# Kernel optimization log

Hardware: AMD Instinct MI355X
Metric: run time of the kernel (lower is better)

## Reference

```python
import jax, jax.numpy as jnp
import numpy as np

B, T, H, W, CIN = 8, 10, 64, 64, 32
F = 64          # filters
KH, KW = 3, 3
G = 4           # num_gate_copies


def _conv(x, k):
    # x: (N,H,W,Cin), k: (kh,kw,Cin,Cout), SAME padding, stride 1
    return jax.lax.conv_general_dilated(
        x, k, window_strides=(1, 1), padding='SAME',
        dimension_numbers=('NHWC', 'HWIO', 'NHWC'))


def setup_inputs() -> dict:
    key = jax.random.key(0)
    k1, k2, k3, k4 = jax.random.split(key, 4)
    inputs = jax.random.normal(k1, (B, T, H, W, CIN), dtype=jnp.float32)
    label_values = jax.random.randint(k2, (B,), 0, G, dtype=jnp.int32)
    kernel = jax.random.normal(k3, (KH, KW, CIN, 4 * F), dtype=jnp.float32) * 0.05
    recurrent_kernel = jax.random.normal(k4, (G, KH, KW, F, 4 * F), dtype=jnp.float32) * 0.05
    # unit_forget_bias: zeros with forget-gate slice set to 1.0
    bias = jnp.zeros((G, 4 * F), dtype=jnp.float32).at[:, F:2 * F].set(1.0)
    return {"inputs": inputs, "label_values": label_values,
            "kernel": kernel, "recurrent_kernel": recurrent_kernel, "bias": bias}


def reference(inputs, label_values, kernel, recurrent_kernel, bias):
    b, t, h_dim, w_dim, _ = inputs.shape
    f = recurrent_kernel.shape[-1] // 4
    # Per-sample gather of expert recurrent kernel / bias (label-indexed)
    k_b = recurrent_kernel[label_values]   # (B, kh, kw, F, 4F)
    b_b = bias[label_values]               # (B, 4F)

    # vmapped per-sample batch=1 recurrent conv (faithful to map_fn semantics)
    per_sample_conv = jax.vmap(lambda hs, ks: _conv(hs[None], ks)[0])

    def step(carry, x_t):
        h, c = carry
        z = _conv(x_t, kernel) + per_sample_conv(h, k_b) + b_b[:, None, None, :]
        i = jax.nn.sigmoid(z[..., :f])
        fg = jax.nn.sigmoid(z[..., f:2 * f])
        g = jnp.tanh(z[..., 2 * f:3 * f])
        o = jax.nn.sigmoid(z[..., 3 * f:])
        c_new = fg * c + i * g
        h_new = o * jnp.tanh(c_new)
        return (h_new, c_new), h_new

    h0 = jnp.zeros((b, h_dim, w_dim, f), dtype=inputs.dtype)
    c0 = jnp.zeros_like(h0)
    xs = jnp.moveaxis(inputs, 1, 0)  # (T, B, H, W, Cin)
    _, ys = jax.lax.scan(step, (h0, c0), xs)
    return jnp.moveaxis(ys, 0, 1)    # (B, T, H, W, F)
```

## Files before the change

kernel.cpp:

```cpp
#include <hip/hip_runtime.h>


typedef __attribute__((ext_vector_type(8))) short short8v;
typedef __attribute__((ext_vector_type(4))) float f32x4;
typedef __attribute__((ext_vector_type(4))) unsigned int u32x4;
typedef unsigned short u16;

#define HS 808
#define HB 3200

__device__ __forceinline__ u16 f2bf(float x) {
    union { float f; unsigned u; } a; a.f = x;
    unsigned r = a.u + 0x7FFFu + ((a.u >> 16) & 1u);
    return (u16)(r >> 16);
}
__device__ __forceinline__ float sigf(float x) { return 1.0f / (1.0f + __expf(-x)); }
__device__ __forceinline__ float tanhf_(float x) {
    float e = __expf(2.0f * x);
    return 1.0f - 2.0f / (e + 1.0f);
}

__global__ __launch_bounds__(256)
void prep_w(const float* __restrict__ kern, const float* __restrict__ rk,
            u16* __restrict__ wt_in, u16* __restrict__ wt_rk,
            unsigned* __restrict__ flags) {
    int idx = blockIdx.x * 256 + threadIdx.x;
    if (idx < 512) flags[idx] = 0u;
    if (idx >= 82944) return;
    const float* s;
    u16* dst;
    if (idx < 9216) {
        int co = idx & 255, ckb = idx >> 8;
        int tap = ckb >> 2, kb = ckb & 3;
        s = kern + (size_t)((tap << 5) + (kb << 3)) * 256 + co;
        dst = wt_in + (size_t)idx * 8;
    } else {
        int j = idx - 9216;
        int co = j & 255, rest = j >> 8;
        int kb = rest & 3, gc = rest >> 2;
        int g = gc / 18, cc = gc - g * 18;
        int tap = cc >> 1;
        int cib = (cc & 1) << 5;
        s = rk + (size_t)(((g * 9 + tap) << 6) + cib + (kb << 3)) * 256 + co;
        dst = wt_rk + (size_t)j * 8;
    }
    union { u16 u[8]; uint4 q; } o;
    #pragma unroll
    for (int i = 0; i < 8; ++i) o.u[i] = f2bf(s[i * 256]);
    *(uint4*)dst = o.q;
}

__device__ __forceinline__ void stageXf(const float* __restrict__ src,
                                        short* __restrict__ halX,
                                        int tid, int y0, int x0) {
    #pragma unroll 2
    for (int s = tid; s < 400; s += 256) {
        int pos = s >> 2, kb = s & 3;
        int hy = pos / 10, hx = pos - hy * 10;
        int gy = y0 + hy - 1, gx = x0 + hx - 1;
        union { u16 u[8]; short8v v; } o;
        o.v = (short8v){0,0,0,0,0,0,0,0};
        if ((unsigned)gy < 64u && (unsigned)gx < 64u) {
            const float* p = src + (((gy << 6) + gx) << 5) + (kb << 3);
            float4 a0 = *(const float4*)p;
            float4 a1 = *(const float4*)(p + 4);
            o.u[0] = f2bf(a0.x); o.u[1] = f2bf(a0.y);
            o.u[2] = f2bf(a0.z); o.u[3] = f2bf(a0.w);
            o.u[4] = f2bf(a1.x); o.u[5] = f2bf(a1.y);
            o.u[6] = f2bf(a1.z); o.u[7] = f2bf(a1.w);
        }
        *(short8v*)&halX[kb * 800 + pos * 8] = o.v;
    }
}

__global__ __launch_bounds__(256, 2)
void lstm_all(const float* __restrict__ xf,
              const u16* __restrict__ wt_in, const u16* __restrict__ wt_rk,
              const float* __restrict__ bias, const int* __restrict__ labels,
              u16* __restrict__ hb0, u16* __restrict__ hb1,
              float* __restrict__ out, unsigned* __restrict__ flags)
{
    __shared__ short hal[HB + 8 * HS];

    const int tid  = threadIdx.x;
    const int lane = tid & 63;
    const int wq   = tid >> 6;
    const int b    = blockIdx.x >> 6;
    const int tile = blockIdx.x & 63;
    const int ty = tile >> 3, tx = tile & 7;
    const int y0 = ty << 3, x0 = tx << 3;
    const int g = labels[b];

    const int co_l = lane & 15;
    const int kbl  = lane >> 4;
    const int prow = (lane & 15) >> 3, pcol = lane & 7;
    const int f = (wq << 4) + co_l;

    float bv[4];
    #pragma unroll
    for (int n = 0; n < 4; ++n)
        bv[n] = bias[(g << 8) + (n << 6) + f];

    int aoffm[4];
    #pragma unroll
    for (int m = 0; m < 4; ++m)
        aoffm[m] = ((m << 1) + prow) * 10 + pcol;

    int poff[4][4], loff[4][4];
    #pragma unroll
    for (int m = 0; m < 4; ++m)
        #pragma unroll
        for (int rr = 0; rr < 4; ++rr) {
            int pf = (kbl << 2) + rr;
            int ly = (m << 1) + (pf >> 3);
            int lx = pf & 7;
            poff[m][rr] = ((((y0 + ly) << 6) + x0 + lx) << 6) + f;
            loff[m][rr] = HB + (f >> 3) * HS + ((ly + 1) * 10 + lx + 1) * 8 + (f & 7);
        }

    float cst[4][4];
    #pragma unroll
    for (int m = 0; m < 4; ++m)
        #pragma unroll
        for (int rr = 0; rr < 4; ++rr) cst[m][rr] = 0.0f;

    const float* xsrc = xf + ((size_t)b * 10 << 17);
    float*       ob0  = out + ((size_t)b * 10 << 18);
    unsigned*    myfl = flags + (b << 6) + tile;

    for (int s = tid; s < 808; s += 256)
        *(short8v*)&hal[HB + s * 8] = (short8v){0,0,0,0,0,0,0,0};
    stageXf(xsrc, hal, tid, y0, x0);
    __syncthreads();

    for (int t = 0; t < 10; ++t) {
        u16* hw = ((t & 1) ? hb1 : hb0) + ((size_t)b << 18);

        f32x4 acc[4][4];
        #pragma unroll
        for (int n = 0; n < 4; ++n)
            #pragma unroll
            for (int m = 0; m < 4; ++m)
                acc[m][n] = (f32x4){bv[n], bv[n], bv[n], bv[n]};

        #pragma unroll 3
        for (int tap = 0; tap < 9; ++tap) {
            const int koff = (tap / 3) * 10 + (tap % 3);
            const u16* wb = wt_in + (size_t)((((tap << 2) + kbl) << 8) + f) * 8;
            short8v bfr[4], af[4];
            #pragma unroll
            for (int n = 0; n < 4; ++n)
                bfr[n] = *(const short8v*)&wb[(size_t)n << 9];
            #pragma unroll
            for (int m = 0; m < 4; ++m)
                af[m] = *(const short8v*)&hal[kbl * 800 + (aoffm[m] + koff) * 8];
            #pragma unroll
            for (int m = 0; m < 4; ++m)
                #pragma unroll
                for (int n = 0; n < 4; ++n)
                    acc[m][n] = __builtin_amdgcn_mfma_f32_16x16x32_bf16(af[m], bfr[n], acc[m][n], 0, 0, 0);
        }

        if (t > 0) {
            if (tid < 64) {
                bool valid = false; int fidx = 0;
                if (tid < 8) {
                    int kk = tid + (tid >= 4);
                    int nty = ty + kk / 3 - 1, ntx = tx + kk % 3 - 1;
                    valid = (unsigned)nty < 8u && (unsigned)ntx < 8u;
                    fidx = (b << 6) + (nty << 3) + ntx;
                }
                unsigned tgt = (unsigned)t;
                int guard = 0;
                for (;;) {
                    unsigned vv = tgt;
                    if (valid)
                        vv = __hip_atomic_load(flags + fidx, __ATOMIC_RELAXED,
                                               __HIP_MEMORY_SCOPE_SYSTEM);
                    if (__all(vv >= tgt)) break;
                    if (++guard > (1 << 19)) break;
                    __builtin_amdgcn_s_sleep(2);
                }
            }
            __syncthreads();

            {
                const u16* hr = ((t & 1) ? hb0 : hb1) + ((size_t)b << 18);
                #pragma unroll
                for (int u = 0; u < 2; ++u) {
                    int s = tid + (u << 8);
                    if (s < 288) {
                        int posr = s >> 3, kb = s & 7;
                        int hy, hx;
                        if (posr < 10)      { hy = 0; hx = posr; }
                        else if (posr < 20) { hy = 9; hx = posr - 10; }
                        else { int v = posr - 20; hy = 1 + (v >> 1); hx = (v & 1) * 9; }
                        int gy = y0 + hy - 1, gx = x0 + hx - 1;
                        bool inb = (unsigned)gy < 64u && (unsigned)gx < 64u;
                        const u16* ga = inb ? (hr + (((gy << 6) + gx) << 6) + (kb << 3)) : hr;
                        u32x4 v;
                        asm volatile("global_load_dwordx4 %0, %1, off sc0 sc1"
                                     : "=v"(v) : "v"(ga) : "memory");
                        asm volatile("s_waitcnt vmcnt(0)" ::: "memory");
                        __builtin_amdgcn_sched_barrier(0);
                        if (!inb) v = (u32x4){0u, 0u, 0u, 0u};
                        *(u32x4*)&hal[HB + kb * HS + (hy * 10 + hx) * 8] = v;
                    }
                }
            }
            __syncthreads();

            #pragma unroll 3
            for (int c = 0; c < 18; ++c) {
                const int tap = c >> 1;
                const int koff = (tap / 3) * 10 + (tap % 3);
                const u16* wb = wt_rk + (size_t)(((((g * 18 + c) << 2) + kbl) << 8) + f) * 8;
                short8v bfr[4], af[4];
                #pragma unroll
                for (int n = 0; n < 4; ++n)
                    bfr[n] = *(const short8v*)&wb[(size_t)n << 9];
                const int abase = HB + (((c & 1) << 2) + kbl) * HS;
                #pragma unroll
                for (int m = 0; m < 4; ++m)
                    af[m] = *(const short8v*)&hal[abase + (aoffm[m] + koff) * 8];
                #pragma unroll
                for (int m = 0; m < 4; ++m)
                    #pragma unroll
                    for (int n = 0; n < 4; ++n)
                        acc[m][n] = __builtin_amdgcn_mfma_f32_16x16x32_bf16(af[m], bfr[n], acc[m][n], 0, 0, 0);
            }
        }
        __syncthreads();

        float* ob = ob0 + ((size_t)t << 18);
        #pragma unroll
        for (int m = 0; m < 4; ++m) {
            #pragma unroll
            for (int rr = 0; rr < 4; ++rr) {
                float zi = acc[m][0][rr], zf = acc[m][1][rr];
                float zg = acc[m][2][rr], zo = acc[m][3][rr];
                float cn = sigf(zf) * cst[m][rr] + sigf(zi) * tanhf_(zg);
                float hn = sigf(zo) * tanhf_(cn);
                cst[m][rr] = cn;
                ob[poff[m][rr]] = hn;
                hal[loff[m][rr]] = (short)f2bf(hn);
            }
        }
        __syncthreads();

        if (t < 9) {
            if (tid < 224) {
                int pxr = tid >> 3, kb = tid & 7;
                int dy, dx;
                if (pxr < 8)       { dy = 0; dx = pxr; }
                else if (pxr < 16) { dy = 7; dx = pxr - 8; }
                else { int v = pxr - 16; dy = 1 + (v >> 1); dx = (v & 1) * 7; }
                u32x4 v = *(const u32x4*)&hal[HB + kb * HS + ((dy + 1) * 10 + dx + 1) * 8];
                const u16* ga = hw + ((((y0 + dy) << 6) + x0 + dx) << 6) + (kb << 3);
                asm volatile("global_store_dwordx4 %0, %1, off sc0 sc1"
                             :: "v"(ga), "v"(v) : "memory");
            }
            stageXf(xsrc + ((size_t)(t + 1) << 17), hal, tid, y0, x0);
            asm volatile("s_waitcnt vmcnt(0)" ::: "memory");
            __syncthreads();
            if (tid == 0)
                __hip_atomic_fetch_add(myfl, 1u, __ATOMIC_RELAXED,
                                       __HIP_MEMORY_SCOPE_SYSTEM);
        }
    }
}

extern "C" void kernel_launch(void* const* d_in, const int* in_sizes, int n_in,
                              void* d_out, int out_size, void* d_ws, size_t ws_size,
                              hipStream_t stream)
{
    const float* x    = (const float*)d_in[0];
    const int*   lbl  = (const int*)  d_in[1];
    const float* kern = (const float*)d_in[2];
    const float* rk   = (const float*)d_in[3];
    const float* bias = (const float*)d_in[4];
    float* out = (float*)d_out;

    u16* hb0   = (u16*)d_ws;
    u16* hb1   = hb0 + 2097152;
    u16* wt_in = hb1 + 2097152;
    u16* wt_rk = wt_in + 73728;
    unsigned* flags = (unsigned*)(wt_rk + 589824);

    hipLaunchKernelGGL(prep_w, dim3(324), dim3(256), 0, stream,
                       kern, rk, wt_in, wt_rk, flags);

    hipLaunchKernelGGL(lstm_all, dim3(512), dim3(256), 0, stream,
                       x, wt_in, wt_rk, bias, lbl, hb0, hb1, out, flags);
}
```

Baseline: 172.1 us.

## Overlap halo neighbor loads with input-conv MFMA taps after flag wait

Splits the input convolution into two chunks and places the flag spin-wait between them. The halo reads of neighbouring h tiles are issued as relaxed atomic 64-bit loads before the last four input taps, so their global latency is hidden behind MFMA work. The old path serialized each load with a vmcnt(0) wait. Halo address offsets are now precomputed once outside the time loop. The risk is that more input-conv work sits after the wait, which could lengthen the critical path if the neighbour flags arrive early.

```diff
diff --git a/kernel.cpp b/kernel.cpp
--- a/kernel.cpp
+++ b/kernel.cpp
@@ -5,6 +5,7 @@
 typedef __attribute__((ext_vector_type(4))) float f32x4;
 typedef __attribute__((ext_vector_type(4))) unsigned int u32x4;
 typedef unsigned short u16;
+typedef unsigned long long u64;
 
 #define HS 808
 #define HB 3200
@@ -73,6 +74,26 @@
     }
 }
 
+__device__ __forceinline__ void xchunk(const u16* __restrict__ wt_in,
+                                       const short* __restrict__ hal,
+                                       f32x4 acc[4][4], const int* aoffm,
+                                       int tap, int kbl, int f) {
+    const int koff = (tap / 3) * 10 + (tap % 3);
+    const u16* wb = wt_in + (size_t)((((tap << 2) + kbl) << 8) + f) * 8;
+    short8v bfr[4], af[4];
+    #pragma unroll
+    for (int n = 0; n < 4; ++n)
+        bfr[n] = *(const short8v*)&wb[(size_t)n << 9];
+    #pragma unroll
+    for (int m = 0; m < 4; ++m)
+        af[m] = *(const short8v*)&hal[kbl * 800 + (aoffm[m] + koff) * 8];
+    #pragma unroll
+    for (int m = 0; m < 4; ++m)
+        #pragma unroll
+        for (int n = 0; n < 4; ++n)
+            acc[m][n] = __builtin_amdgcn_mfma_f32_16x16x32_bf16(af[m], bfr[n], acc[m][n], 0, 0, 0);
+}
+
 __global__ __launch_bounds__(256, 2)
 void lstm_all(const float* __restrict__ xf,
               const u16* __restrict__ wt_in, const u16* __restrict__ wt_rk,
@@ -118,6 +139,32 @@
             loff[m][rr] = HB + (f >> 3) * HS + ((ly + 1) * 10 + lx + 1) * 8 + (f & 7);
         }
 
+    int ilA, ilB = 0;
+    bool inA, inB = false;
+    const bool okB = tid < 32;
+    long offA = 0, offB = 0;
+    {
+        int posr = tid >> 3, kb = tid & 7;
+        int hy, hx;
+        if (posr < 10)      { hy = 0; hx = posr; }
+        else if (posr < 20) { hy = 9; hx = posr - 10; }
+        else { int v = posr - 20; hy = 1 + (v >> 1); hx = (v & 1) * 9; }
+        int gy = y0 + hy - 1, gx = x0 + hx - 1;
+        inA = (unsigned)gy < 64u && (unsigned)gx < 64u;
+        offA = inA ? (long)((((gy << 6) + gx) << 6) + (kb << 3)) : 0;
+        ilA = HB + kb * HS + (hy * 10 + hx) * 8;
+    }
+    if (okB) {
+        int s = tid + 256;
+        int posr = s >> 3, kb = s & 7;
+        int v = posr - 20;
+        int hy = 1 + (v >> 1), hx = (v & 1) * 9;
+        int gy = y0 + hy - 1, gx = x0 + hx - 1;
+        inB = (unsigned)gy < 64u && (unsigned)gx < 64u;
+        offB = inB ? (long)((((gy << 6) + gx) << 6) + (kb << 3)) : 0;
+        ilB = HB + kb * HS + (hy * 10 + hx) * 8;
+    }
+
     float cst[4][4];
     #pragma unroll
     for (int m = 0; m < 4; ++m)
@@ -143,25 +190,15 @@
             for (int m = 0; m < 4; ++m)
                 acc[m][n] = (f32x4){bv[n], bv[n], bv[n], bv[n]};
 
-        #pragma unroll 3
-        for (int tap = 0; tap < 9; ++tap) {
-            const int koff = (tap / 3) * 10 + (tap % 3);
-            const u16* wb = wt_in + (size_t)((((tap << 2) + kbl) << 8) + f) * 8;
-            short8v bfr[4], af[4];
+        if (t == 0) {
+            #pragma unroll 3
+            for (int tap = 0; tap < 9; ++tap)
+                xchunk(wt_in, hal, acc, aoffm, tap, kbl, f);
+        } else {
             #pragma unroll
-            for (int n = 0; n < 4; ++n)
-                bfr[n] = *(const short8v*)&wb[(size_t)n << 9];
-            #pragma unroll
-            for (int m = 0; m < 4; ++m)
-                af[m] = *(const short8v*)&hal[kbl * 800 + (aoffm[m] + koff) * 8];
-            #pragma unroll
-            for (int m = 0; m < 4; ++m)
-                #pragma unroll
-                for (int n = 0; n < 4; ++n)
-                    acc[m][n] = __builtin_amdgcn_mfma_f32_16x16x32_bf16(af[m], bfr[n], acc[m][n], 0, 0, 0);
-        }
-
-        if (t > 0) {
+            for (int tap = 0; tap < 5; ++tap)
+                xchunk(wt_in, hal, acc, aoffm, tap, kbl, f);
+
             if (tid < 64) {
                 bool valid = false; int fidx = 0;
                 if (tid < 8) {
@@ -184,29 +221,32 @@
             }
             __syncthreads();
 
+            const u16* hr = ((t & 1) ? hb0 : hb1) + ((size_t)b << 18);
+            u64 vA0, vA1, vB0 = 0, vB1 = 0;
             {
-                const u16* hr = ((t & 1) ? hb0 : hb1) + ((size_t)b << 18);
-                #pragma unroll
-                for (int u = 0; u < 2; ++u) {
-                    int s = tid + (u << 8);
-                    if (s < 288) {
-                        int posr = s >> 3, kb = s & 7;
-                        int hy, hx;
-                        if (posr < 10)      { hy = 0; hx = posr; }
-                        else if (posr < 20) { hy = 9; hx = posr - 10; }
-                        else { int v = posr - 20; hy = 1 + (v >> 1); hx = (v & 1) * 9; }
-                        int gy = y0 + hy - 1, gx = x0 + hx - 1;
-                        bool inb = (unsigned)gy < 64u && (unsigned)gx < 64u;
-                        const u16* ga = inb ? (hr + (((gy << 6) + gx) << 6) + (kb << 3)) : hr;
-                        u32x4 v;
-                        asm volatile("global_load_dwordx4 %0, %1, off sc0 sc1"
-                                     : "=v"(v) : "v"(ga) : "memory");
-                        asm volatile("s_waitcnt vmcnt(0)" ::: "memory");
-                        __builtin_amdgcn_sched_barrier(0);
-                        if (!inb) v = (u32x4){0u, 0u, 0u, 0u};
-                        *(u32x4*)&hal[HB + kb * HS + (hy * 10 + hx) * 8] = v;
-                    }
-                }
+                const u64* pa = (const u64*)(hr + offA);
+                vA0 = __hip_atomic_load(pa,     __ATOMIC_RELAXED, __HIP_MEMORY_SCOPE_SYSTEM);
+                vA1 = __hip_atomic_load(pa + 1, __ATOMIC_RELAXED, __HIP_MEMORY_SCOPE_SYSTEM);
+            }
+            if (okB) {
+                const u64* pb = (const u64*)(hr + offB);
+                vB0 = __hip_atomic_load(pb,     __ATOMIC_RELAXED, __HIP_MEMORY_SCOPE_SYSTEM);
+                vB1 = __hip_atomic_load(pb + 1, __ATOMIC_RELAXED, __HIP_MEMORY_SCOPE_SYSTEM);
+            }
+
+            #pragma unroll
+            for (int tap = 5; tap < 9; ++tap)
+                xchunk(wt_in, hal, acc, aoffm, tap, kbl, f);
+
+            {
+                u64 a0 = inA ? vA0 : 0ull, a1 = inA ? vA1 : 0ull;
+                *(u64*)&hal[ilA]     = a0;
+                *(u64*)&hal[ilA + 4] = a1;
+            }
+            if (okB) {
+                u64 b0 = inB ? vB0 : 0ull, b1 = inB ? vB1 : 0ull;
+                *(u64*)&hal[ilB]     = b0;
+                *(u64*)&hal[ilB + 4] = b1;
             }
             __syncthreads();
 
```

Measured after the change: 221.0 us. 1.28x slower.

## Split each spatial tile across two blocks by filter half to double grid size

Applied to the files above, without the earlier changes.

Each 8x8 tile is now processed by two blocks, each computing half of the filters (32 of 64). The grid grows from 512 to 1024 blocks and the launch bounds now allow 4 blocks per CU. Each block exchanges its computed h half with the sibling block through global memory, and the flag wait covers the sibling as well as the spatial neighbours. The aim is to spread the recurrent work over more CUs and waves, at the cost of input-conv and staging work duplicated per block, an extra interior-tile h load each step, and more cross-block synchronisation.

```diff
diff --git a/kernel.cpp b/kernel.cpp
--- a/kernel.cpp
+++ b/kernel.cpp
@@ -25,7 +25,7 @@
             u16* __restrict__ wt_in, u16* __restrict__ wt_rk,
             unsigned* __restrict__ flags) {
     int idx = blockIdx.x * 256 + threadIdx.x;
-    if (idx < 512) flags[idx] = 0u;
+    if (idx < 1024) flags[idx] = 0u;
     if (idx >= 82944) return;
     const float* s;
     u16* dst;
@@ -73,7 +73,7 @@
     }
 }
 
-__global__ __launch_bounds__(256, 2)
+__global__ __launch_bounds__(256, 4)
 void lstm_all(const float* __restrict__ xf,
               const u16* __restrict__ wt_in, const u16* __restrict__ wt_rk,
               const float* __restrict__ bias, const int* __restrict__ labels,
@@ -84,9 +84,13 @@
 
     const int tid  = threadIdx.x;
     const int lane = tid & 63;
-    const int wq   = tid >> 6;
-    const int b    = blockIdx.x >> 6;
-    const int tile = blockIdx.x & 63;
+    const int w    = tid >> 6;
+    const int pxh  = w >> 1;
+    const int fq   = w & 1;
+    const int bid  = blockIdx.x;
+    const int fh   = bid & 1;
+    const int tile = (bid >> 1) & 63;
+    const int b    = bid >> 7;
     const int ty = tile >> 3, tx = tile & 7;
     const int y0 = ty << 3, x0 = tx << 3;
     const int g = labels[b];
@@ -94,39 +98,39 @@
     const int co_l = lane & 15;
     const int kbl  = lane >> 4;
     const int prow = (lane & 15) >> 3, pcol = lane & 7;
-    const int f = (wq << 4) + co_l;
+    const int f = (fh << 5) + (fq << 4) + co_l;
 
     float bv[4];
     #pragma unroll
     for (int n = 0; n < 4; ++n)
         bv[n] = bias[(g << 8) + (n << 6) + f];
 
-    int aoffm[4];
-    #pragma unroll
-    for (int m = 0; m < 4; ++m)
-        aoffm[m] = ((m << 1) + prow) * 10 + pcol;
-
-    int poff[4][4], loff[4][4];
-    #pragma unroll
-    for (int m = 0; m < 4; ++m)
+    int aoffm[2];
+    #pragma unroll
+    for (int m = 0; m < 2; ++m)
+        aoffm[m] = ((pxh << 2) + (m << 1) + prow) * 10 + pcol;
+
+    int poff[2][4], loff[2][4];
+    #pragma unroll
+    for (int m = 0; m < 2; ++m)
         #pragma unroll
         for (int rr = 0; rr < 4; ++rr) {
             int pf = (kbl << 2) + rr;
-            int ly = (m << 1) + (pf >> 3);
+            int ly = (pxh << 2) + (m << 1) + (pf >> 3);
             int lx = pf & 7;
             poff[m][rr] = ((((y0 + ly) << 6) + x0 + lx) << 6) + f;
             loff[m][rr] = HB + (f >> 3) * HS + ((ly + 1) * 10 + lx + 1) * 8 + (f & 7);
         }
 
-    float cst[4][4];
-    #pragma unroll
-    for (int m = 0; m < 4; ++m)
+    float cst[2][4];
+    #pragma unroll
+    for (int m = 0; m < 2; ++m)
         #pragma unroll
         for (int rr = 0; rr < 4; ++rr) cst[m][rr] = 0.0f;
 
     const float* xsrc = xf + ((size_t)b * 10 << 17);
     float*       ob0  = out + ((size_t)b * 10 << 18);
-    unsigned*    myfl = flags + (b << 6) + tile;
+    unsigned*    myfl = flags + bid;
 
     for (int s = tid; s < 808; s += 256)
         *(short8v*)&hal[HB + s * 8] = (short8v){0,0,0,0,0,0,0,0};
@@ -136,26 +140,26 @@
     for (int t = 0; t < 10; ++t) {
         u16* hw = ((t & 1) ? hb1 : hb0) + ((size_t)b << 18);
 
-        f32x4 acc[4][4];
+        f32x4 acc[2][4];
         #pragma unroll
         for (int n = 0; n < 4; ++n)
             #pragma unroll
-            for (int m = 0; m < 4; ++m)
+            for (int m = 0; m < 2; ++m)
                 acc[m][n] = (f32x4){bv[n], bv[n], bv[n], bv[n]};
 
         #pragma unroll 3
         for (int tap = 0; tap < 9; ++tap) {
             const int koff = (tap / 3) * 10 + (tap % 3);
             const u16* wb = wt_in + (size_t)((((tap << 2) + kbl) << 8) + f) * 8;
-            short8v bfr[4], af[4];
+            short8v bfr[4], af[2];
             #pragma unroll
             for (int n = 0; n < 4; ++n)
                 bfr[n] = *(const short8v*)&wb[(size_t)n << 9];
             #pragma unroll
-            for (int m = 0; m < 4; ++m)
+            for (int m = 0; m < 2; ++m)
                 af[m] = *(const short8v*)&hal[kbl * 800 + (aoffm[m] + koff) * 8];
             #pragma unroll
-            for (int m = 0; m < 4; ++m)
+            for (int m = 0; m < 2; ++m)
                 #pragma unroll
                 for (int n = 0; n < 4; ++n)
                     acc[m][n] = __builtin_amdgcn_mfma_f32_16x16x32_bf16(af[m], bfr[n], acc[m][n], 0, 0, 0);
@@ -164,11 +168,15 @@
         if (t > 0) {
             if (tid < 64) {
                 bool valid = false; int fidx = 0;
-                if (tid < 8) {
-                    int kk = tid + (tid >= 4);
+                if (tid < 16) {
+                    int k = tid >> 1;
+                    int kk = k + (k >= 4);
                     int nty = ty + kk / 3 - 1, ntx = tx + kk % 3 - 1;
                     valid = (unsigned)nty < 8u && (unsigned)ntx < 8u;
-                    fidx = (b << 6) + (nty << 3) + ntx;
+                    fidx = (b << 7) + ((((nty << 3) + ntx) << 1) | (tid & 1));
+                } else if (tid == 16) {
+                    valid = true;
+                    fidx = (b << 7) + (tile << 1) + (1 - fh);
                 }
                 unsigned tgt = (unsigned)t;
                 int guard = 0;
@@ -184,29 +192,39 @@
             }
             __syncthreads();
 
+            const u16* hr = ((t & 1) ? hb0 : hb1) + ((size_t)b << 18);
+            #pragma unroll
+            for (int u = 0; u < 2; ++u) {
+                int s = tid + (u << 8);
+                if (s < 288) {
+                    int posr = s >> 3, kb = s & 7;
+                    int hy, hx;
+                    if (posr < 10)      { hy = 0; hx = posr; }
+                    else if (posr < 20) { hy = 9; hx = posr - 10; }
+                    else { int v = posr - 20; hy = 1 + (v >> 1); hx = (v & 1) * 9; }
+                    int gy = y0 + hy - 1, gx = x0 + hx - 1;
+                    bool inb = (unsigned)gy < 64u && (unsigned)gx < 64u;
+                    const u16* ga = inb ? (hr + (((gy << 6) + gx) << 6) + (kb << 3)) : hr;
+                    u32x4 v;
+                    asm volatile("global_load_dwordx4 %0, %1, off sc0 sc1"
+                                 : "=v"(v) : "v"(ga) : "memory");
+                    asm volatile("s_waitcnt vmcnt(0)" ::: "memory");
+                    __builtin_amdgcn_sched_barrier(0);
+                    if (!inb) v = (u32x4){0u, 0u, 0u, 0u};
+                    *(u32x4*)&hal[HB + kb * HS + (hy * 10 + hx) * 8] = v;
+                }
+            }
             {
-                const u16* hr = ((t & 1) ? hb0 : hb1) + ((size_t)b << 18);
-                #pragma unroll
-                for (int u = 0; u < 2; ++u) {
-                    int s = tid + (u << 8);
-                    if (s < 288) {
-                        int posr = s >> 3, kb = s & 7;
-                        int hy, hx;
-                        if (posr < 10)      { hy = 0; hx = posr; }
-                        else if (posr < 20) { hy = 9; hx = posr - 10; }
-                        else { int v = posr - 20; hy = 1 + (v >> 1); hx = (v & 1) * 9; }
-                        int gy = y0 + hy - 1, gx = x0 + hx - 1;
-                        bool inb = (unsigned)gy < 64u && (unsigned)gx < 64u;
-                        const u16* ga = inb ? (hr + (((gy << 6) + gx) << 6) + (kb << 3)) : hr;
-                        u32x4 v;
-                        asm volatile("global_load_dwordx4 %0, %1, off sc0 sc1"
-                                     : "=v"(v) : "v"(ga) : "memory");
-                        asm volatile("s_waitcnt vmcnt(0)" ::: "memory");
-                        __builtin_amdgcn_sched_barrier(0);
-                        if (!inb) v = (u32x4){0u, 0u, 0u, 0u};
-                        *(u32x4*)&hal[HB + kb * HS + (hy * 10 + hx) * 8] = v;
-                    }
-                }
+                int px = tid >> 2;
+                int kbu = ((1 - fh) << 2) + (tid & 3);
+                int py = px >> 3, pxx = px & 7;
+                const u16* ga = hr + ((((y0 + py) << 6) + x0 + pxx) << 6) + (kbu << 3);
+                u32x4 v;
+                asm volatile("global_load_dwordx4 %0, %1, off sc0 sc1"
+                             : "=v"(v) : "v"(ga) : "memory");
+                asm volatile("s_waitcnt vmcnt(0)" ::: "memory");
+                __builtin_amdgcn_sched_barrier(0);
+                *(u32x4*)&hal[HB + kbu * HS + ((py + 1) * 10 + pxx + 1) * 8] = v;
             }
             __syncthreads();
 
@@ -215,16 +233,16 @@
                 const int tap = c >> 1;
                 const int koff = (tap / 3) * 10 + (tap % 3);
                 const u16* wb = wt_rk + (size_t)(((((g * 18 + c) << 2) + kbl) << 8) + f) * 8;
-                short8v bfr[4], af[4];
+                short8v bfr[4], af[2];
                 #pragma unroll
                 for (int n = 0; n < 4; ++n)
                     bfr[n] = *(const short8v*)&wb[(size_t)n << 9];
                 const int abase = HB + (((c & 1) << 2) + kbl) * HS;
                 #pragma unroll
-                for (int m = 0; m < 4; ++m)
+                for (int m = 0; m < 2; ++m)
                     af[m] = *(const short8v*)&hal[abase + (aoffm[m] + koff) * 8];
                 #pragma unroll
-                for (int m = 0; m < 4; ++m)
+                for (int m = 0; m < 2; ++m)
                     #pragma unroll
                     for (int n = 0; n < 4; ++n)
                         acc[m][n] = __builtin_amdgcn_mfma_f32_16x16x32_bf16(af[m], bfr[n], acc[m][n], 0, 0, 0);
@@ -234,7 +252,7 @@
 
         float* ob = ob0 + ((size_t)t << 18);
         #pragma unroll
-        for (int m = 0; m < 4; ++m) {
+        for (int m = 0; m < 2; ++m) {
             #pragma unroll
             for (int rr = 0; rr < 4; ++rr) {
                 float zi = acc[m][0][rr], zf = acc[m][1][rr];
@@ -249,14 +267,12 @@
         __syncthreads();
 
         if (t < 9) {
-            if (tid < 224) {
-                int pxr = tid >> 3, kb = tid & 7;
-                int dy, dx;
-                if (pxr < 8)       { dy = 0; dx = pxr; }
-                else if (pxr < 16) { dy = 7; dx = pxr - 8; }
-                else { int v = pxr - 16; dy = 1 + (v >> 1); dx = (v & 1) * 7; }
-                u32x4 v = *(const u32x4*)&hal[HB + kb * HS + ((dy + 1) * 10 + dx + 1) * 8];
-                const u16* ga = hw + ((((y0 + dy) << 6) + x0 + dx) << 6) + (kb << 3);
+            {
+                int px = tid >> 2;
+                int kbu = (fh << 2) + (tid & 3);
+                int py = px >> 3, pxx = px & 7;
+                u32x4 v = *(const u32x4*)&hal[HB + kbu * HS + ((py + 1) * 10 + pxx + 1) * 8];
+                const u16* ga = hw + ((((y0 + py) << 6) + x0 + pxx) << 6) + (kbu << 3);
                 asm volatile("global_store_dwordx4 %0, %1, off sc0 sc1"
                              :: "v"(ga), "v"(v) : "memory");
             }
@@ -290,6 +306,6 @@
     hipLaunchKernelGGL(prep_w, dim3(324), dim3(256), 0, stream,
                        kern, rk, wt_in, wt_rk, flags);
 
-    hipLaunchKernelGGL(lstm_all, dim3(512), dim3(256), 0, stream,
+    hipLaunchKernelGGL(lstm_all, dim3(1024), dim3(256), 0, stream,
                        x, wt_in, wt_rk, bias, lbl, hb0, hb1, out, flags);
 }
```

After: 202.3 us. 17.5% more time.
